# Optimization experiments

Measured on AMD Instinct MI355X. Metric: run time of the kernel, lower is better.

The kernel has to match this reference:

```python
import jax, jax.numpy as jnp
import numpy as np


def dense_image_warp(img, flow):
    """Faithful port of tfa.image.dense_image_warp(img, flow):
    output[b,i,j] = bilinear_sample(img[b], (i - flow[b,i,j,0], j - flow[b,i,j,1]))
    with floors clamped to [0, size-2] and alphas clipped to [0,1] (TFA semantics).
    """
    B, H, W, C = img.shape
    gy = jnp.arange(H, dtype=flow.dtype)[None, :, None]   # [1,H,1]
    gx = jnp.arange(W, dtype=flow.dtype)[None, None, :]   # [1,1,W]
    # query = grid - flow
    qy = gy - flow[..., 0]                                 # [B,H,W]
    qx = gx - flow[..., 1]
    fy = jnp.clip(jnp.floor(qy), 0.0, H - 2)
    fx = jnp.clip(jnp.floor(qx), 0.0, W - 2)
    ay = jnp.clip(qy - fy, 0.0, 1.0)[..., None]            # [B,H,W,1]
    ax = jnp.clip(qx - fx, 0.0, 1.0)[..., None]
    fy_i = fy.astype(jnp.int32)
    fx_i = fx.astype(jnp.int32)

    flat = img.reshape(B, H * W, C)

    def gather(yy, xx):  # yy,xx: [B,H,W] int32
        idx = (yy * W + xx).reshape(B, H * W, 1)
        return jnp.take_along_axis(flat, idx, axis=1).reshape(B, H, W, C)

    tl = gather(fy_i,     fx_i)
    tr = gather(fy_i,     fx_i + 1)
    bl = gather(fy_i + 1, fx_i)
    br = gather(fy_i + 1, fx_i + 1)

    top = tl + (tr - tl) * ax
    bot = bl + (br - bl) * ax
    return top + (bot - top) * ay


def setup_inputs() -> dict:
    key = jax.random.key(0)
    k1, k2 = jax.random.split(key)
    img = jax.random.normal(k1, (16, 256, 512, 32), dtype=jnp.float32)
    flow = jax.random.normal(k2, (16, 256, 512, 2), dtype=jnp.float32)
    return {"img": img, "flow": flow}


def reference(img, flow):
    # InvWarpFlow.call: dense_image_warp(img, -flow)
    return dense_image_warp(img, -flow)
```

## Files before the change

kernel.cpp:

```cpp
#include <hip/hip_runtime.h>


typedef float floatx4 __attribute__((ext_vector_type(4)));

__global__ __launch_bounds__(512) void InvWarpFlow_kernel(
    const float* __restrict__ img,
    const float* __restrict__ flow,
    float* __restrict__ out)
{
    constexpr int H = 256, W = 512, C = 32;
    constexpr int TW = 8, TH = 8;
    constexpr int TILES_Y = H / TH;
    constexpr int TILES_X = W / TW;
    constexpr int NBLK = 16 * TILES_X * TILES_Y;
    constexpr int PER_XCD = NBLK / 8;

    int bid = blockIdx.x;
    int logical = (bid & 7) * PER_XCD + (bid >> 3);

    int ty   = logical & (TILES_Y - 1);
    int rest = logical >> 5;
    int tx   = rest & (TILES_X - 1);
    int b    = rest >> 6;

    int t  = threadIdx.x;
    int cg = t & 7;
    int p  = t >> 3;
    int lx = p & 7;
    int ly = p >> 3;

    int x = tx * TW + lx;
    int y = ty * TH + ly;
    int pix = ((b << 8) + y) * W + x;

    const float2 f = *reinterpret_cast<const float2*>(flow + (size_t)pix * 2);
    float qy = (float)y + f.x;
    float qx = (float)x + f.y;

    float fy = fminf(fmaxf(floorf(qy), 0.0f), (float)(H - 2));
    float fx = fminf(fmaxf(floorf(qx), 0.0f), (float)(W - 2));
    float ay = fminf(fmaxf(qy - fy, 0.0f), 1.0f);
    float ax = fminf(fmaxf(qx - fx, 0.0f), 1.0f);
    int iy = (int)fy;
    int ix = (int)fx;

    const float* base = img + ((((size_t)b * H + iy) * W + ix) * C) + cg * 4;
    floatx4 tl = *reinterpret_cast<const floatx4*>(base);
    floatx4 tr = *reinterpret_cast<const floatx4*>(base + C);
    floatx4 bl = *reinterpret_cast<const floatx4*>(base + (size_t)W * C);
    floatx4 br = *reinterpret_cast<const floatx4*>(base + (size_t)W * C + C);

    floatx4 top = tl + (tr - tl) * ax;
    floatx4 bot = bl + (br - bl) * ax;
    floatx4 o   = top + (bot - top) * ay;

    __builtin_nontemporal_store(o, reinterpret_cast<floatx4*>(out + (size_t)pix * C + cg * 4));
}

extern "C" void kernel_launch(void* const* d_in, const int* in_sizes, int n_in,
                              void* d_out, int out_size, void* d_ws, size_t ws_size,
                              hipStream_t stream) {
    const float* img  = (const float*)d_in[0];
    const float* flow = (const float*)d_in[1];
    float* out = (float*)d_out;

    constexpr int NBLK = 32768;
    InvWarpFlow_kernel<<<NBLK, 512, 0, stream>>>(img, flow, out);
}
```

Measured before the change: 117.3 us.

## Process four pixels per thread with batched gathers and larger tiles

Each thread now handles four vertically adjacent pixels. It issues all sixteen gather loads before doing any interpolation, which raises memory-level parallelism per thread. The tile becomes 8x16 with 256-thread blocks, and the block-to-tile mapping now runs x-fastest, which changes how tiles are assigned across XCDs and so affects L2 locality. The trade-off is more registers per thread and fewer total threads.

```diff
diff --git a/kernel.cpp b/kernel.cpp
--- a/kernel.cpp
+++ b/kernel.cpp
@@ -3,58 +3,70 @@
 
 typedef float floatx4 __attribute__((ext_vector_type(4)));
 
-__global__ __launch_bounds__(512) void InvWarpFlow_kernel(
+__global__ __launch_bounds__(256) void InvWarpFlow_kernel(
     const float* __restrict__ img,
     const float* __restrict__ flow,
     float* __restrict__ out)
 {
     constexpr int H = 256, W = 512, C = 32;
-    constexpr int TW = 8, TH = 8;
+    constexpr int TW = 8, TH = 16;
+    constexpr int TILES_X = W / TW;
     constexpr int TILES_Y = H / TH;
-    constexpr int TILES_X = W / TW;
     constexpr int NBLK = 16 * TILES_X * TILES_Y;
     constexpr int PER_XCD = NBLK / 8;
 
     int bid = blockIdx.x;
     int logical = (bid & 7) * PER_XCD + (bid >> 3);
 
-    int ty   = logical & (TILES_Y - 1);
-    int rest = logical >> 5;
-    int tx   = rest & (TILES_X - 1);
-    int b    = rest >> 6;
+    int tx = logical & (TILES_X - 1);
+    int r  = logical >> 6;
+    int ty = r & (TILES_Y - 1);
+    int b  = r >> 4;
 
     int t  = threadIdx.x;
     int cg = t & 7;
-    int p  = t >> 3;
-    int lx = p & 7;
-    int ly = p >> 3;
+    int s  = t >> 3;
+    int lx = s & 7;
+    int wv = s >> 3;
 
-    int x = tx * TW + lx;
-    int y = ty * TH + ly;
-    int pix = ((b << 8) + y) * W + x;
+    int x  = tx * TW + lx;
+    int y0 = ty * TH + wv * 4;
+    int pix0 = ((b << 8) + y0) * W + x;
 
-    const float2 f = *reinterpret_cast<const float2*>(flow + (size_t)pix * 2);
-    float qy = (float)y + f.x;
-    float qx = (float)x + f.y;
+    float2 f[4];
+    #pragma unroll
+    for (int k = 0; k < 4; ++k)
+        f[k] = *reinterpret_cast<const float2*>(flow + (size_t)(pix0 + k * W) * 2);
 
-    float fy = fminf(fmaxf(floorf(qy), 0.0f), (float)(H - 2));
-    float fx = fminf(fmaxf(floorf(qx), 0.0f), (float)(W - 2));
-    float ay = fminf(fmaxf(qy - fy, 0.0f), 1.0f);
-    float ax = fminf(fmaxf(qx - fx, 0.0f), 1.0f);
-    int iy = (int)fy;
-    int ix = (int)fx;
+    const float* ib = img + (size_t)b * H * W * C + cg * 4;
 
-    const float* base = img + ((((size_t)b * H + iy) * W + ix) * C) + cg * 4;
-    floatx4 tl = *reinterpret_cast<const floatx4*>(base);
-    floatx4 tr = *reinterpret_cast<const floatx4*>(base + C);
-    floatx4 bl = *reinterpret_cast<const floatx4*>(base + (size_t)W * C);
-    floatx4 br = *reinterpret_cast<const floatx4*>(base + (size_t)W * C + C);
+    floatx4 tl[4], tr[4], bl[4], br[4];
+    float ax[4], ay[4];
+    #pragma unroll
+    for (int k = 0; k < 4; ++k) {
+        float qy = (float)(y0 + k) + f[k].x;
+        float qx = (float)x + f[k].y;
+        float fy = fminf(fmaxf(floorf(qy), 0.0f), (float)(H - 2));
+        float fx = fminf(fmaxf(floorf(qx), 0.0f), (float)(W - 2));
+        ay[k] = fminf(fmaxf(qy - fy, 0.0f), 1.0f);
+        ax[k] = fminf(fmaxf(qx - fx, 0.0f), 1.0f);
+        int iy = (int)fy;
+        int ix = (int)fx;
+        const float* base = ib + ((size_t)iy * W + ix) * C;
+        tl[k] = *reinterpret_cast<const floatx4*>(base);
+        tr[k] = *reinterpret_cast<const floatx4*>(base + C);
+        bl[k] = *reinterpret_cast<const floatx4*>(base + (size_t)W * C);
+        br[k] = *reinterpret_cast<const floatx4*>(base + (size_t)W * C + C);
+    }
 
-    floatx4 top = tl + (tr - tl) * ax;
-    floatx4 bot = bl + (br - bl) * ax;
-    floatx4 o   = top + (bot - top) * ay;
-
-    __builtin_nontemporal_store(o, reinterpret_cast<floatx4*>(out + (size_t)pix * C + cg * 4));
+    #pragma unroll
+    for (int k = 0; k < 4; ++k) {
+        floatx4 top = tl[k] + (tr[k] - tl[k]) * ax[k];
+        floatx4 bot = bl[k] + (br[k] - bl[k]) * ax[k];
+        floatx4 o   = top + (bot - top) * ay[k];
+        __builtin_nontemporal_store(
+            o, reinterpret_cast<floatx4*>(out + (size_t)(pix0 + k * W) * C + cg * 4));
+    }
 }
 
 extern "C" void kernel_launch(void* const* d_in, const int* in_sizes, int n_in,
@@ -64,6 +76,6 @@
     const float* flow = (const float*)d_in[1];
     float* out = (float*)d_out;
 
-    constexpr int NBLK = 32768;
-    InvWarpFlow_kernel<<<NBLK, 512, 0, stream>>>(img, flow, out);
+    constexpr int NBLK = 16384;
+    InvWarpFlow_kernel<<<NBLK, 256, 0, stream>>>(img, flow, out);
 }
```

Result: faster. 111.9 us (-4.6%).

## Stage haloed image band in LDS via async global_load_lds for bilinear gathers

Applied to the files above, without the earlier changes.

Each block now covers a 16x16 pixel tile and first copies a 24x24 haloed image patch plus the tile's flow into LDS using global_load_lds. The four bilinear taps are then read from LDS, with a fallback to global memory when a sample lands outside the patch. Each thread loops over 8 pixels, and the launch drops to 8192 blocks of 256 threads. This is meant to turn scattered global gathers into coalesced bulk loads with reuse, at the cost of a 72KB LDS footprint that limits occupancy, extra halo traffic, and a full wait before any compute starts.

```diff
diff --git a/kernel.cpp b/kernel.cpp
--- a/kernel.cpp
+++ b/kernel.cpp
@@ -2,59 +2,105 @@
 
 
 typedef float floatx4 __attribute__((ext_vector_type(4)));
+typedef float floatx2 __attribute__((ext_vector_type(2)));
 
-__global__ __launch_bounds__(512) void InvWarpFlow_kernel(
+__global__ __launch_bounds__(256) void InvWarpFlow_kernel(
     const float* __restrict__ img,
     const float* __restrict__ flow,
     float* __restrict__ out)
 {
     constexpr int H = 256, W = 512, C = 32;
-    constexpr int TW = 8, TH = 8;
-    constexpr int TILES_Y = H / TH;
+    constexpr int TW = 16, RPT = 16;
+    constexpr int BW = 24, NR = 24;
     constexpr int TILES_X = W / TW;
+    constexpr int TILES_Y = H / RPT;
     constexpr int NBLK = 16 * TILES_X * TILES_Y;
     constexpr int PER_XCD = NBLK / 8;
 
+    __shared__ float simg[NR * BW * 32];
+    __shared__ float sflow[RPT * TW * 2];
+
     int bid = blockIdx.x;
     int logical = (bid & 7) * PER_XCD + (bid >> 3);
+    int tx = logical & (TILES_X - 1);
+    int r  = logical >> 5;
+    int ty = r & (TILES_Y - 1);
+    int b  = r >> 4;
 
-    int ty   = logical & (TILES_Y - 1);
-    int rest = logical >> 5;
-    int tx   = rest & (TILES_X - 1);
-    int b    = rest >> 6;
+    int x0 = tx * TW;
+    int y0 = ty * RPT;
+    int by0 = min(max(y0 - 4, 0), H - NR);
+    int bx0 = min(max(x0 - 4, 0), W - BW);
 
-    int t  = threadIdx.x;
-    int cg = t & 7;
-    int p  = t >> 3;
-    int lx = p & 7;
-    int ly = p >> 3;
+    int t = threadIdx.x;
 
-    int x = tx * TW + lx;
-    int y = ty * TH + ly;
-    int pix = ((b << 8) + y) * W + x;
+    {
+        const float* gband = img + (((size_t)(b * H + by0)) * W + bx0) * C;
+        #pragma unroll
+        for (int it = 0; it < 18; ++it) {
+            int o16 = it * 256 + t;
+            int row = o16 / 192;
+            int w16 = o16 - row * 192;
+            const float* src = gband + (size_t)row * (W * C) + w16 * 4;
+            float* dst = simg + (size_t)(it * 256 + (t & ~63)) * 4;
+            __builtin_amdgcn_global_load_lds(
+                (const __attribute__((address_space(1))) float*)src,
+                (__attribute__((address_space(3))) float*)dst, 16, 0, 0);
+        }
+    }
+    if (t < 128) {
+        int row = t >> 3;
+        int w16 = t & 7;
+        const float* src = flow + (((size_t)(b * H + y0 + row)) * W + x0 + w16 * 2) * 2;
+        float* dst = sflow + (size_t)(t & ~63) * 4;
+        __builtin_amdgcn_global_load_lds(
+            (const __attribute__((address_space(1))) float*)src,
+            (__attribute__((address_space(3))) float*)dst, 16, 0, 0);
+    }
 
-    const float2 f = *reinterpret_cast<const float2*>(flow + (size_t)pix * 2);
-    float qy = (float)y + f.x;
-    float qx = (float)x + f.y;
+    asm volatile("s_waitcnt vmcnt(0)" ::: "memory");
+    __syncthreads();
 
-    float fy = fminf(fmaxf(floorf(qy), 0.0f), (float)(H - 2));
-    float fx = fminf(fmaxf(floorf(qx), 0.0f), (float)(W - 2));
-    float ay = fminf(fmaxf(qy - fy, 0.0f), 1.0f);
-    float ax = fminf(fmaxf(qx - fx, 0.0f), 1.0f);
-    int iy = (int)fy;
-    int ix = (int)fx;
+    int cg   = t & 7;
+    int px   = (t >> 3) & 15;
+    int half = t >> 7;
+    int x    = x0 + px;
 
-    const float* base = img + ((((size_t)b * H + iy) * W + ix) * C) + cg * 4;
-    floatx4 tl = *reinterpret_cast<const floatx4*>(base);
-    floatx4 tr = *reinterpret_cast<const floatx4*>(base + C);
-    floatx4 bl = *reinterpret_cast<const floatx4*>(base + (size_t)W * C);
-    floatx4 br = *reinterpret_cast<const floatx4*>(base + (size_t)W * C + C);
+    #pragma unroll
+    for (int k = 0; k < 8; ++k) {
+        int yrow = half * 8 + k;
+        int y = y0 + yrow;
+        floatx2 f = *reinterpret_cast<const floatx2*>(sflow + (yrow * TW + px) * 2);
+        float qy = (float)y + f.x;
+        float qx = (float)x + f.y;
+        float fy = fminf(fmaxf(floorf(qy), 0.0f), (float)(H - 2));
+        float fx = fminf(fmaxf(floorf(qx), 0.0f), (float)(W - 2));
+        float ay = fminf(fmaxf(qy - fy, 0.0f), 1.0f);
+        float ax = fminf(fmaxf(qx - fx, 0.0f), 1.0f);
+        int iy = (int)fy;
+        int ix = (int)fx;
 
-    floatx4 top = tl + (tr - tl) * ax;
-    floatx4 bot = bl + (br - bl) * ax;
-    floatx4 o   = top + (bot - top) * ay;
+        floatx4 tl, tr, bl, br;
+        if (iy >= by0 && iy <= by0 + NR - 2 && ix >= bx0 && ix <= bx0 + BW - 2) {
+            const float* p = simg + ((size_t)(iy - by0) * BW + (ix - bx0)) * 32 + cg * 4;
+            tl = *reinterpret_cast<const floatx4*>(p);
+            tr = *reinterpret_cast<const floatx4*>(p + 32);
+            bl = *reinterpret_cast<const floatx4*>(p + BW * 32);
+            br = *reinterpret_cast<const floatx4*>(p + BW * 32 + 32);
+        } else {
+            const float* g = img + (((size_t)(b * H + iy)) * W + ix) * C + cg * 4;
+            tl = *reinterpret_cast<const floatx4*>(g);
+            tr = *reinterpret_cast<const floatx4*>(g + C);
+            bl = *reinterpret_cast<const floatx4*>(g + (size_t)W * C);
+            br = *reinterpret_cast<const floatx4*>(g + (size_t)W * C + C);
+        }
 
-    __builtin_nontemporal_store(o, reinterpret_cast<floatx4*>(out + (size_t)pix * C + cg * 4));
+        floatx4 top = tl + (tr - tl) * ax;
+        floatx4 bot = bl + (br - bl) * ax;
+        floatx4 o   = top + (bot - top) * ay;
+        __builtin_nontemporal_store(
+            o, reinterpret_cast<floatx4*>(out + (((size_t)(b * H + y)) * W + x) * C + cg * 4));
+    }
 }
 
 extern "C" void kernel_launch(void* const* d_in, const int* in_sizes, int n_in,
@@ -64,6 +110,6 @@
     const float* flow = (const float*)d_in[1];
     float* out = (float*)d_out;
 
-    constexpr int NBLK = 32768;
-    InvWarpFlow_kernel<<<NBLK, 512, 0, stream>>>(img, flow, out);
+    constexpr int NBLK = 8192;
+    InvWarpFlow_kernel<<<NBLK, 256, 0, stream>>>(img, flow, out);
 }
```

Result: faster. 111.2 us (-5.2%).
